# Optimization experiments

Measured on AMD Instinct MI355X. Metric: run time of the kernel, lower is better.

Reference implementation:

```python
import jax, jax.numpy as jnp
import numpy as np
from jax import lax

K = 8            # number of object slots
H = 250          # hidden / fc_size
EPS = 1e-5
DN = ('NCHW', 'OIHW', 'NCHW')


def ln_all(x):
    # F.layer_norm over all non-batch dims, no affine params (torch init: w=1,b=0)
    ax = tuple(range(1, x.ndim))
    m = jnp.mean(x, ax, keepdims=True)
    v = jnp.var(x, ax, keepdims=True)
    return (x - m) * lax.rsqrt(v + EPS)


def ln_last(x):
    # nn.LayerNorm(feat) -> last dim only
    m = jnp.mean(x, -1, keepdims=True)
    v = jnp.var(x, -1, keepdims=True)
    return (x - m) * lax.rsqrt(v + EPS)


def conv(x, w, b):
    # torch Conv2d(k=4, s=2, p=1), NCHW
    y = lax.conv_general_dilated(x, w, (2, 2), [(1, 1), (1, 1)], dimension_numbers=DN)
    return y + b[None, :, None, None]


def up4(x):
    return jnp.repeat(jnp.repeat(x, 4, axis=2), 4, axis=3)


def setup_inputs():
    ks = jax.random.split(jax.random.key(0), 20)
    bk = 48 * K
    p = lambda i, shape, s: jax.random.normal(ks[i], shape, jnp.float32) * s
    z = lambda n: jnp.zeros((n,), jnp.float32)
    return dict(
        x=p(0, (bk, 4096), 1.0),
        state=p(1, (bk, H), 1.0),
        # encoder convs (OIHW) + fc
        c1w=p(2, (16, 1, 4, 4), 0.25), c1b=z(16),
        c2w=p(3, (32, 16, 4, 4), 0.06), c2b=z(32),
        c3w=p(4, (64, 32, 4, 4), 0.04), c3b=z(64),
        efc_w=p(5, (4096, 512), 0.016), efc_b=z(512),
        # R_NEM (weights stored as [in, out])
        renc_w=p(6, (H, H), 0.06), renc_b=z(H),
        core_w=p(7, (2 * H, H), 0.045), core_b=z(H),
        ctx_w=p(8, (H, H), 0.06), ctx_b=z(H),
        att1_w=p(9, (H, 100), 0.06), att1_b=z(100),
        att2_w=p(10, (100, 1), 0.1), att2_b=z(1),
        out_w=p(11, (2 * H + 512, H), 0.03), out_b=z(H),
        # decoder fcs + convs
        dfc1_w=p(12, (H, 512), 0.06), dfc1_b=z(512),
        dfc2_w=p(13, (512, 4096), 0.045), dfc2_b=z(4096),
        d1w=p(14, (32, 64, 4, 4), 0.03), d1b=z(32),
        d2w=p(15, (16, 32, 4, 4), 0.045), d2b=z(16),
        d3w=p(16, (1, 16, 4, 4), 0.06), d3b=z(1),
    )


def reference(x, state, c1w, c1b, c2w, c2b, c3w, c3b, efc_w, efc_b,
              renc_w, renc_b, core_w, core_b, ctx_w, ctx_b,
              att1_w, att1_b, att2_w, att2_b, out_w, out_b,
              dfc1_w, dfc1_b, dfc2_w, dfc2_b, d1w, d1b, d2w, d2b, d3w, d3b):
    bk = x.shape[0]
    b = bk // K

    # ---------------- EncoderLayer ----------------
    def inwrap(h, w, bias):  # InputWrapper conv branch: NHWC -> permute(0,3,2,1) -> conv -> back
        y = conv(jnp.transpose(h, (0, 3, 2, 1)), w, bias)
        return jax.nn.elu(ln_all(jnp.transpose(y, (0, 3, 2, 1))))

    h = x.reshape(bk, 64, 64, 1)
    h = inwrap(h, c1w, c1b)                 # (bk,32,32,16)
    h = inwrap(h, c2w, c2b)                 # (bk,16,16,32)
    h = inwrap(h, c3w, c3b)                 # (bk,8,8,64)
    h = h.reshape(bk, -1)                   # (bk,4096)
    h = jax.nn.elu(ln_last(h @ efc_w + efc_b))   # (bk,512)

    # ---------------- R_NEM (RecurrentLayer) ----------------
    s1 = jax.nn.relu(ln_last(state @ renc_w + renc_b))   # (bk,H)
    s1r = s1.reshape(b, K, H)
    idx = np.array([[j for j in range(K) if j != i] for i in range(K)])  # (K,K-1)
    cs = s1r[:, idx, :]                                    # context: (b,K,K-1,H)
    fs = jnp.broadcast_to(s1r[:, :, None, :], cs.shape)    # focus copies
    pair = jnp.concatenate([fs, cs], axis=-1)              # (b,K,K-1,2H)
    core = jax.nn.relu(ln_last(pair @ core_w + core_b))    # (b,K,K-1,H)
    ctx = jax.nn.relu(ln_last(core @ ctx_w + ctx_b))       # (b,K,K-1,H)
    att = jax.nn.sigmoid(jnp.tanh(ln_last(core @ att1_w + att1_b)) @ att2_w + att2_b)  # (b,K,K-1,1)
    effect = jnp.sum(ctx * att, axis=2).reshape(bk, H)     # attention-weighted sum over K-1
    total = jnp.concatenate([s1, effect, h], axis=1)       # (bk, 2H+512)
    new_state = total @ out_w + out_b                      # (bk,H)
    xr = jax.nn.sigmoid(ln_last(new_state))
    state_out = jax.nn.sigmoid(new_state)

    # ---------------- DecoderLayer ----------------
    d = jax.nn.relu(ln_last(xr @ dfc1_w + dfc1_b))         # (bk,512)
    d = jax.nn.relu(ln_last(d @ dfc2_w + dfc2_b))          # (bk,4096)
    d = d.reshape(bk, 8, 8, 64)

    def outwrap(t, w, bias):
        y = conv(up4(jnp.transpose(t, (0, 3, 2, 1))), w, bias)
        return jnp.transpose(y, (0, 3, 2, 1))

    d = jax.nn.relu(ln_all(outwrap(d, d1w, d1b)))          # (bk,16,16,32)
    d = jax.nn.relu(ln_all(outwrap(d, d2w, d2b)))          # (bk,32,32,16)
    d = jax.nn.sigmoid(outwrap(d, d3w, d3b))               # (bk,64,64,1), no LN
    x_out = d.reshape(bk, -1)                              # (bk,4096)
    return x_out, state_out
```

## Files before the change

### kernel.cpp

```cpp
#include <hip/hip_runtime.h>
#include <hip/hip_bf16.h>
#include <math.h>

typedef __attribute__((ext_vector_type(8))) short bf16x8;
typedef __attribute__((ext_vector_type(4))) float f32x4;

__device__ __forceinline__ float eluf(float v){ return v > 0.f ? v : expm1f(v); }
__device__ __forceinline__ float sigf(float v){ return 1.f/(1.f+expf(-v)); }
__device__ __forceinline__ unsigned short f2bf(float f){
  unsigned u = __float_as_uint(f);
  u += 0x7FFFu + ((u >> 16) & 1u);
  return (unsigned short)(u >> 16);
}
__device__ __forceinline__ float bf2f(short s){
  return __uint_as_float(((unsigned)(unsigned short)s) << 16);
}

__device__ __forceinline__ void block_reduce2(float& a, float& b, float* sbuf){
  __syncthreads();
  for (int off = 32; off; off >>= 1){
    a += __shfl_down(a, off);
    b += __shfl_down(b, off);
  }
  int lane = threadIdx.x & 63, w = threadIdx.x >> 6;
  if (lane == 0){ sbuf[2*w] = a; sbuf[2*w+1] = b; }
  __syncthreads();
  if (threadIdx.x == 0){
    int nw = blockDim.x >> 6;
    float sa = 0.f, sb = 0.f;
    for (int i = 0; i < nw; i++){ sa += sbuf[2*i]; sb += sbuf[2*i+1]; }
    sbuf[0] = sa; sbuf[1] = sb;
  }
  __syncthreads();
  a = sbuf[0]; b = sbuf[1];
}

__device__ __forceinline__ float fold_sum(const float* __restrict__ w, int O, int I,
                                          int o, int i, int pa, int pb, int da, int db){
  float s = 0.f;
  for (int kh = 0; kh < 4; kh++){
    bool inh = (pb==0) ? (db==0 ? (kh==0) : (kh>=1)) : (db==0 ? (kh<=2) : (kh==3));
    if (!inh) continue;
    for (int kw = 0; kw < 4; kw++){
      bool inw = (pa==0) ? (da==0 ? (kw==0) : (kw>=1)) : (da==0 ? (kw<=2) : (kw==3));
      if (!inw) continue;
      s += w[((o*I + i)*4 + kh)*4 + kw];
    }
  }
  return s;
}
__device__ __forceinline__ void fold_elem(const float* __restrict__ w, float* __restrict__ CW,
                                          int O, int I, int l){
  int o = l % O; int q = l / O;
  int da = q & 1, db = (q>>1)&1, pa = (q>>2)&1, pb = (q>>3)&1, i = q>>4;
  CW[(((pb*2+pa)*4 + db*2+da)*I + i)*O + o] = fold_sum(w, O, I, o, i, pa, pb, da, db);
}
__device__ __forceinline__ void cvtc2_elem(const float* __restrict__ w, short* __restrict__ D, int l){
  int i = l & 15, t = (l>>4) & 15, o = l>>8;
  D[l] = (short)f2bf(w[(o*16 + i)*16 + t]);
}
__device__ __forceinline__ void cvtc3_elem(const float* __restrict__ w, short* __restrict__ D, int l){
  int i = l & 31, t = (l>>5) & 15, o = l>>9;
  D[l] = (short)f2bf(w[(o*32 + i)*16 + t]);
}
__device__ __forceinline__ void foldd1_elem(const float* __restrict__ w, short* __restrict__ D, int l){
  int i = l & 63, tap = (l>>6)&3, o = (l>>8)&31, ph = l>>13;
  D[l] = (short)f2bf(fold_sum(w, 32, 64, o, i, ph&1, ph>>1, tap&1, tap>>1));
}
__device__ __forceinline__ void foldd2_elem(const float* __restrict__ w, short* __restrict__ D, int l){
  int i = l & 31, tap = (l>>5)&3, o = (l>>7)&15, ph = l>>11;
  D[l] = (short)f2bf(fold_sum(w, 16, 32, o, i, ph&1, ph>>1, tap&1, tap>>1));
}

__global__ __launch_bounds__(256) void prep_combined(
  const float* __restrict__ efc,  short* __restrict__ Defc,
  const float* __restrict__ dfc2, short* __restrict__ Ddfc2,
  const float* __restrict__ outw, short* __restrict__ Dout,
  const float* __restrict__ corew,short* __restrict__ Dcore,
  const float* __restrict__ dfc1, short* __restrict__ Ddfc1,
  const float* __restrict__ renc, short* __restrict__ Drenc,
  const float* __restrict__ ctx,  const float* __restrict__ att1,
  short* __restrict__ Dctxatt,
  const float* __restrict__ d3w, float* __restrict__ CWT3,
  const float* __restrict__ c2w, short* __restrict__ BtC2,
  const float* __restrict__ c3w, short* __restrict__ BtC3,
  const float* __restrict__ d1w, short* __restrict__ BD1,
  const float* __restrict__ d2w, short* __restrict__ BD2,
  const float* __restrict__ state, short* __restrict__ SBF,
  short* __restrict__ TOTb)
{
  int bx = blockIdx.x;
  if (bx >= 1192){
    const int F3=256, P2=F3+8192, P3=P2+32768, P4=P3+32768, P5=P4+8192,
              ST=P5+98304, TP=ST+4608, TOTAL=TP+8704;
    for (int l = (bx-1192)*256 + threadIdx.x; l < TOTAL; l += 256*256){
      if (l < F3)      fold_elem(d3w, CWT3, 1, 16, l);
      else if (l < P2) cvtc2_elem(c2w, BtC2, l - F3);
      else if (l < P3) cvtc3_elem(c3w, BtC3, l - P2);
      else if (l < P4) foldd1_elem(d1w, BD1, l - P3);
      else if (l < P5) foldd2_elem(d2w, BD2, l - P4);
      else if (l < ST){
        int q = l - P5;
        int n = q >> 8, k = q & 255;
        SBF[q] = (k < 250) ? (short)f2bf(state[n*250 + k]) : (short)0;
      } else if (l < TP){
        int q = l - ST;
        int row = q / 12, cc = q % 12;
        int col = cc < 6 ? 250 + cc : 506 + (cc - 6);
        TOTb[row*1024 + col] = 0;
      } else {
        int q = l - TP;
        int r = q >> 8, cc = q & 255;
        int row = r < 6 ? 250 + r : 356 + (r - 6);
        Dctxatt[row*256 + cc] = 0;
      }
    }
    return;
  }
  const float* W; short* D; int K, N, Kp, base, mode = 0;
  if      (bx < 512) { W=efc;  D=Defc;  K=4096; N=512;  Kp=4096; base=0;    }
  else if (bx < 1024){ W=dfc2; D=Ddfc2; K=512;  N=4096; Kp=512;  base=512;  }
  else if (bx < 1088){ W=outw; D=Dout;  K=1012; N=250;  Kp=1024; base=1024; mode=2; }
  else if (bx < 1120){ W=corew;D=Dcore; K=500;  N=250;  Kp=512;  base=1088; mode=1; }
  else if (bx < 1152){ W=dfc1; D=Ddfc1; K=250;  N=512;  Kp=256;  base=1120; }
  else if (bx < 1168){ W=renc; D=Drenc; K=250;  N=250;  Kp=256;  base=1152; }
  else if (bx < 1184){ W=ctx;  D=Dctxatt;         K=250; N=250; Kp=256; base=1168; }
  else               { W=att1; D=Dctxatt + 65536; K=250; N=100; Kp=256; base=1184; }
  int t = bx - base;
  int tpr = Kp >> 6;
  int tk = t % tpr, tn = t / tpr;
  __shared__ short tile[64][65];
  int c = threadIdx.x & 63, r4 = threadIdx.x >> 6;
  int n0 = tn*64, k0 = tk*64;
  #pragma unroll 4
  for (int p = 0; p < 16; p++){
    int r = r4*16 + p;
    int k = k0 + r, n = n0 + c;
    int ksrc = k; bool valid;
    if (mode == 0) valid = (k < K);
    else if (mode == 1){ valid = (k < 250) || (k >= 256 && k < 506); ksrc = k < 256 ? k : k - 6; }
    else { valid = (k < 250) || (k >= 256 && k < 506) || (k >= 512);
           ksrc = k < 256 ? k : (k < 512 ? k - 6 : k - 12); }
    float v = (valid && n < N) ? W[(size_t)ksrc*N + n] : 0.f;
    tile[c][r] = (short)f2bf(v);
  }
  __syncthreads();
  #pragma unroll 4
  for (int p = 0; p < 16; p++){
    int nn = r4*16 + p;
    int n = n0 + nn;
    if (n < N) D[(size_t)n*Kp + k0 + c] = tile[nn][c];
  }
}

__global__ __launch_bounds__(256) void gemm_mfma(
    const short* __restrict__ Ab, const short* __restrict__ Bt,
    float* __restrict__ P, int M, int N, int Kp, int Kc)
{
  __shared__ __align__(16) short As[64*32];
  __shared__ __align__(16) short Bs[64*32];
  int tid = threadIdx.x;
  int bm = blockIdx.y*64, bn = blockIdx.x*64;
  int kb = blockIdx.z * Kc;
  int kend = kb + Kc;

  int r = tid >> 2, c = tid & 3;
  const short* Arow = Ab + (size_t)(bm + r)*Kp;
  int gn = bn + r;
  bool bval = gn < N;
  const short* Brow = Bt + (size_t)gn*Kp;

  uint4 hA, hB;
  auto load_regs = [&](int k0){
    hA = *(const uint4*)&Arow[k0 + c*8];
    hB = bval ? *(const uint4*)&Brow[k0 + c*8] : make_uint4(0,0,0,0);
  };
  auto write_lds = [&](){
    *(uint4*)&As[r*32 + c*8] = hA;
    *(uint4*)&Bs[r*32 + c*8] = hB;
  };

  int wave = tid >> 6;
  int ln = tid & 15, quad = (tid >> 4) & 3;
  int wr = (wave >> 1) * 32, wc = (wave & 1) * 32;

  f32x4 zero = {0.f, 0.f, 0.f, 0.f};
  f32x4 acc[2][2] = {{zero, zero}, {zero, zero}};

  load_regs(kb);
  write_lds();
  __syncthreads();
  for (int k0 = kb; k0 < kend; k0 += 32){
    int nxt = k0 + 32;
    if (nxt < kend) load_regs(nxt);
    bf16x8 a0 = *(const bf16x8*)&As[(wr +      ln)*32 + quad*8];
    bf16x8 a1 = *(const bf16x8*)&As[(wr + 16 + ln)*32 + quad*8];
    bf16x8 b0 = *(const bf16x8*)&Bs[(wc +      ln)*32 + quad*8];
    bf16x8 b1 = *(const bf16x8*)&Bs[(wc + 16 + ln)*32 + quad*8];
    acc[0][0] = __builtin_amdgcn_mfma_f32_16x16x32_bf16(a0, b0, acc[0][0], 0, 0, 0);
    acc[0][1] = __builtin_amdgcn_mfma_f32_16x16x32_bf16(a0, b1, acc[0][1], 0, 0, 0);
    acc[1][0] = __builtin_amdgcn_mfma_f32_16x16x32_bf16(a1, b0, acc[1][0], 0, 0, 0);
    acc[1][1] = __builtin_amdgcn_mfma_f32_16x16x32_bf16(a1, b1, acc[1][1], 0, 0, 0);
    __syncthreads();
    if (nxt < kend){ write_lds(); __syncthreads(); }
  }

  float* Pout = P + (size_t)blockIdx.z*M*N;
  #pragma unroll
  for (int t = 0; t < 2; t++)
    #pragma unroll
    for (int u = 0; u < 2; u++)
      #pragma unroll
      for (int j = 0; j < 4; j++){
        int row = bm + wr + t*16 + quad*4 + j;
        int col = bn + wc + u*16 + ln;
        if (col < N) Pout[(size_t)row*N + col] = acc[t][u][j];
      }
}

__global__ __launch_bounds__(256) void gemm_conv2g(
    const short* __restrict__ In, const short* __restrict__ Bt,
    short* __restrict__ Out)
{
  __shared__ __align__(16) short As[128*32];
  __shared__ __align__(16) short Bs[32*32];
  int tid = threadIdx.x;
  int bm = blockIdx.x*128;

  int ra = tid >> 1, ca = (tid & 1)*16;
  int gr = bm + ra;
  int n = gr >> 8, pos = gr & 255;
  int oa = pos >> 4, ob = pos & 15;
  const short* ibase = In + (size_t)n*16384;
  int rb = tid >> 2, cb = (tid & 3)*8;
  const short* Brow = Bt + rb*256;
  bool bact = tid < 128;

  uint4 hA0, hA1, hB;
  auto load_regs = [&](int k0){
    #pragma unroll
    for (int h = 0; h < 2; h++){
      int k = k0 + ca + h*8;
      int tap = k >> 4;
      int ai = 2*oa + (tap & 3) - 1, bi = 2*ob + (tap >> 2) - 1;
      bool v = ((unsigned)ai < 32u) && ((unsigned)bi < 32u);
      uint4 tv = v ? *(const uint4*)&ibase[ai*512 + bi*16 + (k & 15)] : make_uint4(0,0,0,0);
      if (h == 0) hA0 = tv; else hA1 = tv;
    }
    if (bact) hB = *(const uint4*)&Brow[k0 + cb];
  };
  auto write_lds = [&](){
    *(uint4*)&As[ra*32 + ca] = hA0;
    *(uint4*)&As[ra*32 + ca + 8] = hA1;
    if (bact) *(uint4*)&Bs[rb*32 + cb] = hB;
  };

  int wave = tid >> 6, ln = tid & 15, quad = (tid >> 4) & 3;
  int wr = wave * 32;

  f32x4 zero = {0.f,0.f,0.f,0.f};
  f32x4 acc[2][2] = {{zero,zero},{zero,zero}};
  load_regs(0); write_lds(); __syncthreads();
  for (int k0 = 0; k0 < 256; k0 += 32){
    int nxt = k0 + 32;
    if (nxt < 256) load_regs(nxt);
    bf16x8 a0 = *(const bf16x8*)&As[(wr +      ln)*32 + quad*8];
    bf16x8 a1 = *(const bf16x8*)&As[(wr + 16 + ln)*32 + quad*8];
    bf16x8 b0 = *(const bf16x8*)&Bs[(     ln)*32 + quad*8];
    bf16x8 b1 = *(const bf16x8*)&Bs[(16 + ln)*32 + quad*8];
    acc[0][0] = __builtin_amdgcn_mfma_f32_16x16x32_bf16(a0, b0, acc[0][0], 0, 0, 0);
    acc[0][1] = __builtin_amdgcn_mfma_f32_16x16x32_bf16(a0, b1, acc[0][1], 0, 0, 0);
    acc[1][0] = __builtin_amdgcn_mfma_f32_16x16x32_bf16(a1, b0, acc[1][0], 0, 0, 0);
    acc[1][1] = __builtin_amdgcn_mfma_f32_16x16x32_bf16(a1, b1, acc[1][1], 0, 0, 0);
    __syncthreads();
    if (nxt < 256){ write_lds(); __syncthreads(); }
  }
  #pragma unroll
  for (int t = 0; t < 2; t++)
    #pragma unroll
    for (int u = 0; u < 2; u++)
      #pragma unroll
      for (int j = 0; j < 4; j++){
        int row = bm + wr + t*16 + quad*4 + j;
        int col = u*16 + ln;
        Out[(size_t)row*32 + col] = (short)f2bf(acc[t][u][j]);
      }
}

__global__ __launch_bounds__(256) void enc_conv3_full(
    const short* __restrict__ E2raw, const float* __restrict__ bias2,
    const short* __restrict__ Bt3, const float* __restrict__ bias3,
    short* __restrict__ outp)
{
  __shared__ __align__(16) short lsamp[18*18*40];
  __shared__ float sbuf[16];
  int n = blockIdx.x, tid = threadIdx.x;
  const short* ip = E2raw + (size_t)n*8192;
  float vv[32];
  float s = 0.f, s2 = 0.f;
  #pragma unroll
  for (int t = 0; t < 4; t++){
    bf16x8 v8 = *(const bf16x8*)&ip[(t*256 + tid)*8];
    #pragma unroll
    for (int j = 0; j < 8; j++){
      int e = (t*256 + tid)*8 + j;
      float v = bf2f(v8[j]) + bias2[e & 31];
      vv[t*8+j] = v; s += v; s2 += v*v;
    }
  }
  block_reduce2(s, s2, sbuf);
  float m2 = s*(1.f/8192.f);
  float rs2 = rsqrtf(s2*(1.f/8192.f) - m2*m2 + 1e-5f);
  for (int l = tid; l < 18*18*40/4; l += 256) ((unsigned long long*)lsamp)[l] = 0ull;
  __syncthreads();
  #pragma unroll
  for (int t = 0; t < 4; t++){
    int e0 = (t*256 + tid)*8;
    int slot = e0 >> 5, ch0 = e0 & 31;
    int a = slot >> 4, b = slot & 15;
    bf16x8 o8;
    #pragma unroll
    for (int j = 0; j < 8; j++)
      o8[j] = (short)f2bf(eluf((vv[t*8+j]-m2)*rs2));
    *(bf16x8*)&lsamp[((a+1)*18 + (b+1))*40 + ch0] = o8;
  }
  int wave = tid>>6, ln = tid&15, quad = (tid>>4)&3;
  int o3 = wave*16 + ln;
  bf16x8 bfr3[16];
  {
    const short* Brow = Bt3 + o3*512;
    #pragma unroll
    for (int ks = 0; ks < 16; ks++)
      bfr3[ks] = *(const bf16x8*)&Brow[ks*32 + quad*8];
  }
  __syncthreads();
  f32x4 z = {0.f,0.f,0.f,0.f};
  f32x4 acc3[4] = {z,z,z,z};
  #pragma unroll
  for (int ks = 0; ks < 16; ks++){
    int kh = ks>>2, kw = ks&3;
    #pragma unroll
    for (int mt = 0; mt < 4; mt++){
      int p = mt*16 + ln;
      int oa = p>>3, ob = p&7;
      bf16x8 a = *(const bf16x8*)&lsamp[((2*oa+kw)*18 + (2*ob+kh))*40 + quad*8];
      acc3[mt] = __builtin_amdgcn_mfma_f32_16x16x32_bf16(a, bfr3[ks], acc3[mt],0,0,0);
    }
  }
  s = 0.f; s2 = 0.f;
  float bz3 = bias3[o3];
  #pragma unroll
  for (int mt = 0; mt < 4; mt++)
    #pragma unroll
    for (int j = 0; j < 4; j++){
      float v = acc3[mt][j] + bz3;
      acc3[mt][j] = v; s += v; s2 += v*v;
    }
  block_reduce2(s, s2, sbuf);
  float m3 = s*(1.f/4096.f);
  float rs3 = rsqrtf(s2*(1.f/4096.f) - m3*m3 + 1e-5f);
  short* op = outp + (size_t)n*4096;
  #pragma unroll
  for (int mt = 0; mt < 4; mt++)
    #pragma unroll
    for (int j = 0; j < 4; j++){
      int p = mt*16 + quad*4 + j;
      int oa = p>>3, ob = p&7;
      op[oa*512 + ob*64 + o3] = f2bf(eluf((acc3[mt][j]-m3)*rs3));
    }
}

__global__ __launch_bounds__(256) void gemm_core_mfma(
    const short* __restrict__ Tb, const short* __restrict__ Bt,
    float* __restrict__ P, int M, int N, int Kc)
{
  __shared__ __align__(16) short As[64*32];
  __shared__ __align__(16) short Bs[64*32];
  int tid = threadIdx.x;
  int bm = blockIdx.y*64, bn = blockIdx.x*64;
  int kb = blockIdx.z * Kc;
  int kend = kb + Kc;

  int r = tid >> 2, c = tid & 3;
  int gr = bm + r;
  int jj2 = gr % 7, fi2 = gr / 7;
  int ii = fi2 & 7, j2 = fi2 >> 3;
  int jidx = jj2 < ii ? jj2 : jj2 + 1;
  const short* own = Tb + (size_t)fi2*1024;
  const short* oth = Tb + (size_t)(j2*8 + jidx)*1024;
  int gn = bn + r;
  bool bval = gn < N;
  const short* Brow = Bt + (size_t)gn*512;

  uint4 hA, hB;
  auto load_regs = [&](int k0){
    int kk = k0 + c*8;
    const short* src = (kk & 256) ? oth : own;
    hA = *(const uint4*)&src[kk & 255];
    hB = bval ? *(const uint4*)&Brow[kk] : make_uint4(0,0,0,0);
  };
  auto write_lds = [&](){
    *(uint4*)&As[r*32 + c*8] = hA;
    *(uint4*)&Bs[r*32 + c*8] = hB;
  };

  int wave = tid >> 6;
  int ln = tid & 15, quad = (tid >> 4) & 3;
  int wr = (wave >> 1) * 32, wc = (wave & 1) * 32;

  f32x4 zero = {0.f, 0.f, 0.f, 0.f};
  f32x4 acc[2][2] = {{zero, zero}, {zero, zero}};

  load_regs(kb);
  write_lds();
  __syncthreads();
  for (int k0 = kb; k0 < kend; k0 += 32){
    int nxt = k0 + 32;
    if (nxt < kend) load_regs(nxt);
    bf16x8 a0 = *(const bf16x8*)&As[(wr +      ln)*32 + quad*8];
    bf16x8 a1 = *(const bf16x8*)&As[(wr + 16 + ln)*32 + quad*8];
    bf16x8 b0 = *(const bf16x8*)&Bs[(wc +      ln)*32 + quad*8];
    bf16x8 b1 = *(const bf16x8*)&Bs[(wc + 16 + ln)*32 + quad*8];
    acc[0][0] = __builtin_amdgcn_mfma_f32_16x16x32_bf16(a0, b0, acc[0][0], 0, 0, 0);
    acc[0][1] = __builtin_amdgcn_mfma_f32_16x16x32_bf16(a0, b1, acc[0][1], 0, 0, 0);
    acc[1][0] = __builtin_amdgcn_mfma_f32_16x16x32_bf16(a1, b0, acc[1][0], 0, 0, 0);
    acc[1][1] = __builtin_amdgcn_mfma_f32_16x16x32_bf16(a1, b1, acc[1][1], 0, 0, 0);
    __syncthreads();
    if (nxt < kend){ write_lds(); __syncthreads(); }
  }

  float* Pout = P + (size_t)blockIdx.z*M*N;
  #pragma unroll
  for (int t = 0; t < 2; t++)
    #pragma unroll
    for (int u = 0; u < 2; u++)
      #pragma unroll
      for (int j = 0; j < 4; j++){
        int row = bm + wr + t*16 + quad*4 + j;
        int col = bn + wc + u*16 + ln;
        if (col < N) Pout[(size_t)row*N + col] = acc[t][u][j];
      }
}

__global__ __launch_bounds__(256) void reduce_ln(
    const float* __restrict__ Pp, const float* __restrict__ bias,
    void* __restrict__ outp, int M, int N, int KS, int os, int act, int obf, int bmask)
{
  __shared__ float rowbuf[4096];
  __shared__ float sbuf[16];
  int row = blockIdx.x;
  size_t MN = (size_t)M*N;
  float s = 0.f, s2 = 0.f;
  for (int c = threadIdx.x; c < N; c += 256){
    float v = bias[c & bmask];
    for (int ks = 0; ks < KS; ks++) v += Pp[ks*MN + (size_t)row*N + c];
    rowbuf[c] = v; s += v; s2 += v*v;
  }
  block_reduce2(s, s2, sbuf);
  float m = s / N;
  float r = rsqrtf(s2/N - m*m + 1e-5f);
  for (int c = threadIdx.x; c < N; c += 256){
    float v = (rowbuf[c]-m)*r;
    if (act == 1) v = fmaxf(v, 0.f);
    else if (act == 2) v = eluf(v);
    else if (act == 3) v = tanhf(v);
    if (obf) ((short*)outp)[(size_t)row*os + c] = f2bf(v);
    else     ((float*)outp)[(size_t)row*os + c] = v;
  }
}

__global__ __launch_bounds__(256) void reduce_ns(
    const float* __restrict__ Pp, const float* __restrict__ bias,
    short* __restrict__ XRb, float* __restrict__ so, int M, int N, int KS)
{
  __shared__ float rowbuf[256];
  __shared__ float sbuf[16];
  int row = blockIdx.x;
  size_t MN = (size_t)M*N;
  float s = 0.f, s2 = 0.f;
  for (int c = threadIdx.x; c < N; c += 256){
    float v = bias[c];
    for (int ks = 0; ks < KS; ks++) v += Pp[ks*MN + (size_t)row*N + c];
    rowbuf[c] = v; s += v; s2 += v*v;
  }
  block_reduce2(s, s2, sbuf);
  float m = s / N;
  float r = rsqrtf(s2/N - m*m + 1e-5f);
  for (int c = threadIdx.x; c < N; c += 256){
    float v = rowbuf[c];
    XRb[(size_t)row*256 + c] = f2bf(sigf((v-m)*r));
    so[(size_t)row*N + c] = sigf(v);
  }
}

__global__ __launch_bounds__(448) void ctx_att_effect(
    const float* __restrict__ Pc, const float* __restrict__ ctx_b,
    const float* __restrict__ att1_b,
    const float* __restrict__ w2, const float* __restrict__ b2,
    short* __restrict__ tot)
{
  __shared__ float ctxs[7][250];
  __shared__ float att_s[7];
  int fi = blockIdx.x, tid = threadIdx.x;
  int jj = tid >> 6, lane = tid & 63;
  const size_t MN = (size_t)2688*384;
  int row = fi*7 + jj;
  float vv[4];
  float s = 0.f, s2 = 0.f;
  #pragma unroll
  for (int t = 0; t < 4; t++){
    int c = lane + t*64;
    float v = 0.f;
    if (c < 250) v = ctx_b[c] + Pc[(size_t)row*384 + c] + Pc[MN + (size_t)row*384 + c];
    vv[t] = v; s += v; s2 += v*v;
  }
  #pragma unroll
  for (int off = 32; off; off >>= 1){ s += __shfl_down(s, off); s2 += __shfl_down(s2, off); }
  s = __shfl(s, 0); s2 = __shfl(s2, 0);
  float m = s*(1.f/250.f);
  float r = rsqrtf(s2*(1.f/250.f) - m*m + 1e-5f);
  #pragma unroll
  for (int t = 0; t < 4; t++){
    int c = lane + t*64;
    if (c < 250) ctxs[jj][c] = fmaxf((vv[t]-m)*r, 0.f);
  }
  float va[2];
  s = 0.f; s2 = 0.f;
  #pragma unroll
  for (int t = 0; t < 2; t++){
    int c = lane + t*64;
    float v = 0.f;
    if (c < 100)
      v = att1_b[c] + Pc[(size_t)row*384 + 256 + c] + Pc[MN + (size_t)row*384 + 256 + c];
    va[t] = v; s += v; s2 += v*v;
  }
  #pragma unroll
  for (int off = 32; off; off >>= 1){ s += __shfl_down(s, off); s2 += __shfl_down(s2, off); }
  s = __shfl(s, 0); s2 = __shfl(s2, 0);
  m = s*0.01f;
  r = rsqrtf(s2*0.01f - m*m + 1e-5f);
  float d = 0.f;
  #pragma unroll
  for (int t = 0; t < 2; t++){
    int c = lane + t*64;
    if (c < 100) d += tanhf((va[t]-m)*r)*w2[c];
  }
  #pragma unroll
  for (int off = 32; off; off >>= 1) d += __shfl_down(d, off);
  if (lane == 0) att_s[jj] = sigf(d + b2[0]);
  __syncthreads();
  for (int h = tid; h < 250; h += 448){
    float sum = 0.f;
    #pragma unroll
    for (int q = 0; q < 7; q++) sum += ctxs[q][h]*att_s[q];
    tot[(size_t)fi*1024 + 256 + h] = f2bf(sum);
  }
}

__global__ __launch_bounds__(256) void enc_conv1_ig(
    const float* __restrict__ x, const float* __restrict__ w, const float* __restrict__ bias,
    short* __restrict__ outp)
{
  __shared__ __align__(16) float in_t[66*68];
  __shared__ short rawb[16384];
  __shared__ float sbuf[16];
  int n = blockIdx.x, tid = threadIdx.x;
  for (int l = tid; l < 66*68; l += 256) in_t[l] = 0.f;
  __syncthreads();
  const float* xin = x + (size_t)n*4096;
  for (int l4 = tid; l4 < 1024; l4 += 256){
    float4 v = *(const float4*)&xin[l4*4];
    int aa = (l4*4) >> 6, bb = (l4*4) & 63;
    float* dst = &in_t[(aa+1)*68 + bb + 1];
    dst[0]=v.x; dst[1]=v.y; dst[2]=v.z; dst[3]=v.w;
  }
  int o = tid & 15;
  float wr[16];
  #pragma unroll
  for (int t = 0; t < 16; t++) wr[t] = w[o*16 + t];
  float bv = bias[o];
  __syncthreads();
  float s = 0.f, s2 = 0.f;
  for (int r = 0; r < 64; r++){
    int idx = tid + (r<<8);
    int bq = (idx>>4)&31, aq = idx>>9;
    int a0 = 2*aq, b0 = 2*bq;
    float acc = bv;
    #pragma unroll
    for (int kw = 0; kw < 4; kw++){
      const float* row = &in_t[(a0+kw)*68 + b0];
      float2 p0 = *(const float2*)&row[0];
      float2 p1 = *(const float2*)&row[2];
      acc += p0.x*wr[0*4+kw] + p0.y*wr[1*4+kw] + p1.x*wr[2*4+kw] + p1.y*wr[3*4+kw];
    }
    rawb[idx] = f2bf(acc);
    s += acc; s2 += acc*acc;
  }
  block_reduce2(s, s2, sbuf);
  float m = s*(1.f/16384.f);
  float rs = rsqrtf(s2*(1.f/16384.f) - m*m + 1e-5f);
  short* op = outp + (size_t)n*16384;
  for (int l = tid; l < 16384; l += 256){
    float v = bf2f(rawb[l]);
    op[l] = f2bf(eluf((v-m)*rs));
  }
}

__global__ __launch_bounds__(256) void dec_conv12_mfma(
    const short* __restrict__ in, const short* __restrict__ Bd1, const float* __restrict__ bias1,
    const short* __restrict__ Bd2, const float* __restrict__ bias2, short* __restrict__ outp)
{
  __shared__ __align__(16) short smem[18*18*40];
  __shared__ float sbuf[16];
  int n = blockIdx.x, tid = threadIdx.x;
  for (int l = tid; l < 1800; l += 256) ((unsigned long long*)smem)[l] = 0ull;
  __syncthreads();
  const short* ip = in + (size_t)n*4096;
  for (int l = tid; l < 1024; l += 256){
    int i4 = l & 15, sb = (l>>4)&7, sa = l>>7;
    *(uint2*)&smem[((sa+1)*10 + (sb+1))*72 + i4*4] = *(const uint2*)&ip[sa*512 + sb*64 + i4*4];
  }
  int wave = tid>>6, ln = tid&15, quad = (tid>>4)&3;
  int pa = wave & 1, pb = wave >> 1;
  bf16x8 bfr1[2][8];
  #pragma unroll
  for (int nt = 0; nt < 2; nt++){
    const short* Brow = Bd1 + (wave*32 + nt*16 + ln)*256;
    #pragma unroll
    for (int ks = 0; ks < 8; ks++)
      bfr1[nt][ks] = *(const bf16x8*)&Brow[ks*32 + quad*8];
  }
  __syncthreads();
  f32x4 z = {0.f,0.f,0.f,0.f};
  f32x4 acc[2][4] = {{z,z,z,z},{z,z,z,z}};
  #pragma unroll
  for (int ks = 0; ks < 8; ks++){
    int tap = ks>>1, ibase = (ks&1)*32 + quad*8;
    int da = tap & 1, db = tap >> 1;
    #pragma unroll
    for (int mt = 0; mt < 4; mt++){
      int p = mt*16 + ln;
      int ta = p>>3, tb = p&7;
      bf16x8 a = *(const bf16x8*)&smem[((ta+da+pa)*10 + (tb+db+pb))*72 + ibase];
      acc[0][mt] = __builtin_amdgcn_mfma_f32_16x16x32_bf16(a, bfr1[0][ks], acc[0][mt],0,0,0);
      acc[1][mt] = __builtin_amdgcn_mfma_f32_16x16x32_bf16(a, bfr1[1][ks], acc[1][mt],0,0,0);
    }
  }
  float s = 0.f, s2 = 0.f;
  #pragma unroll
  for (int nt = 0; nt < 2; nt++){
    float bz = bias1[nt*16 + ln];
    #pragma unroll
    for (int mt = 0; mt < 4; mt++)
      #pragma unroll
      for (int j = 0; j < 4; j++){
        float v = acc[nt][mt][j] + bz;
        acc[nt][mt][j] = v; s += v; s2 += v*v;
      }
  }
  block_reduce2(s, s2, sbuf);
  float m1 = s*(1.f/8192.f);
  float rs1 = rsqrtf(s2*(1.f/8192.f) - m1*m1 + 1e-5f);
  bf16x8 bfr2[4];
  {
    const short* Brow = Bd2 + (wave*16 + ln)*128;
    #pragma unroll
    for (int ks = 0; ks < 4; ks++)
      bfr2[ks] = *(const bf16x8*)&Brow[ks*32 + quad*8];
  }
  for (int l = tid; l < 3240; l += 256) ((unsigned long long*)smem)[l] = 0ull;
  __syncthreads();
  #pragma unroll
  for (int nt = 0; nt < 2; nt++){
    int o = nt*16 + ln;
    #pragma unroll
    for (int mt = 0; mt < 4; mt++)
      #pragma unroll
      for (int j = 0; j < 4; j++){
        int p = mt*16 + quad*4 + j;
        int ta = p>>3, tb = p&7;
        int sa = 2*ta + pa, sb = 2*tb + pb;
        smem[((sa+1)*18 + (sb+1))*40 + o] = f2bf(fmaxf((acc[nt][mt][j]-m1)*rs1, 0.f));
      }
  }
  __syncthreads();
  f32x4 acc2[16] = {z,z,z,z,z,z,z,z,z,z,z,z,z,z,z,z};
  #pragma unroll
  for (int ks = 0; ks < 4; ks++){
    int da = ks & 1, db = ks >> 1;
    #pragma unroll
    for (int mt = 0; mt < 16; mt++){
      int p = mt*16 + ln;
      int ta = p>>4, tb = p&15;
      bf16x8 a = *(const bf16x8*)&smem[((ta+da+pa)*18 + (tb+db+pb))*40 + quad*8];
      acc2[mt] = __builtin_amdgcn_mfma_f32_16x16x32_bf16(a, bfr2[ks], acc2[mt],0,0,0);
    }
  }
  s = 0.f; s2 = 0.f;
  float bz2 = bias2[ln];
  #pragma unroll
  for (int mt = 0; mt < 16; mt++)
    #pragma unroll
    for (int j = 0; j < 4; j++){
      float v = acc2[mt][j] + bz2;
      acc2[mt][j] = v; s += v; s2 += v*v;
    }
  block_reduce2(s, s2, sbuf);
  float m = s*(1.f/16384.f);
  float rs = rsqrtf(s2*(1.f/16384.f) - m*m + 1e-5f);
  short* op = outp + (size_t)n*16384;
  #pragma unroll
  for (int mt = 0; mt < 16; mt++)
    #pragma unroll
    for (int j = 0; j < 4; j++){
      int p = mt*16 + quad*4 + j;
      int ta = p>>4, tb = p&15;
      op[(2*ta+pa)*512 + (2*tb+pb)*16 + ln] = f2bf(fmaxf((acc2[mt][j]-m)*rs, 0.f));
    }
}

__global__ __launch_bounds__(256) void dec_conv3_ig(
    const short* __restrict__ in, const float* __restrict__ CWT, const float* __restrict__ bias,
    float* __restrict__ outp)
{
  __shared__ __align__(16) float in_t[9792];
  __shared__ __align__(16) float wl[256];
  int bx = blockIdx.x;
  int n = bx >> 1, b0 = (bx & 1) * 32, tb0 = b0 >> 1;
  int tid = threadIdx.x;
  const short* ip = in + (size_t)n*16384;
  for (int l = tid; l < 9792; l += 256){
    int i = l & 15, sb = (l >> 4) % 18, sap = l / 288;
    int sa = sap - 1, sbg = tb0 - 1 + sb;
    float v = 0.f;
    if ((unsigned)sa < 32u && (unsigned)sbg < 32u)
      v = bf2f(ip[sa*512 + sbg*16 + i]);
    in_t[(sap*18 + sb)*16 + i] = v;
  }
  for (int l = tid; l < 256; l += 256) wl[l] = CWT[l];
  __syncthreads();
  float bv = bias[0];
  int bl = tid & 31, ath = tid >> 5;
  int b = b0 + bl;
  int tb = b >> 1, pb = b & 1;
  float* op = outp + (size_t)n*4096;
  #pragma unroll
  for (int j = 0; j < 8; j++){
    int a = ath*8 + j;
    int ta = a >> 1, pa = a & 1;
    float4 s4 = make_float4(0.f,0.f,0.f,0.f);
    #pragma unroll
    for (int db = 0; db < 2; db++){
      int sb = tb + db + (pb ? 0 : -1);
      int sbl = sb - (tb0 - 1);
      #pragma unroll
      for (int da = 0; da < 2; da++){
        int sa = ta + da + (pa ? 0 : -1);
        int sap = sa + 1;
        const float4* A4 = (const float4*)&in_t[(sap*18 + sbl)*16];
        const float4* B4 = (const float4*)&wl[((pb*2+pa)*4 + db*2+da)*16];
        #pragma unroll
        for (int q = 0; q < 4; q++){
          float4 av = A4[q], bw = B4[q];
          s4.x += av.x*bw.x; s4.y += av.y*bw.y;
          s4.z += av.z*bw.z; s4.w += av.w*bw.w;
        }
      }
    }
    op[a*64 + b] = sigf(bv + s4.x + s4.y + s4.z + s4.w);
  }
}

extern "C" void kernel_launch(void* const* d_in, const int* in_sizes, int n_in,
                              void* d_out, int out_size, void* d_ws, size_t ws_size,
                              hipStream_t stream) {
  const float* x      = (const float*)d_in[0];
  const float* state  = (const float*)d_in[1];
  const float* c1w    = (const float*)d_in[2];
  const float* c1b    = (const float*)d_in[3];
  const float* c2w    = (const float*)d_in[4];
  const float* c2b    = (const float*)d_in[5];
  const float* c3w    = (const float*)d_in[6];
  const float* c3b    = (const float*)d_in[7];
  const float* efc_w  = (const float*)d_in[8];
  const float* efc_b  = (const float*)d_in[9];
  const float* renc_w = (const float*)d_in[10];
  const float* renc_b = (const float*)d_in[11];
  const float* core_w = (const float*)d_in[12];
  const float* core_b = (const float*)d_in[13];
  const float* ctx_w  = (const float*)d_in[14];
  const float* ctx_b  = (const float*)d_in[15];
  const float* att1_w = (const float*)d_in[16];
  const float* att1_b = (const float*)d_in[17];
  const float* att2_w = (const float*)d_in[18];
  const float* att2_b = (const float*)d_in[19];
  const float* out_w  = (const float*)d_in[20];
  const float* out_b  = (const float*)d_in[21];
  const float* dfc1_w = (const float*)d_in[22];
  const float* dfc1_b = (const float*)d_in[23];
  const float* dfc2_w = (const float*)d_in[24];
  const float* dfc2_b = (const float*)d_in[25];
  const float* d1w    = (const float*)d_in[26];
  const float* d1b    = (const float*)d_in[27];
  const float* d2w    = (const float*)d_in[28];
  const float* d2b    = (const float*)d_in[29];
  const float* d3w    = (const float*)d_in[30];
  const float* d3b    = (const float*)d_in[31];

  float* wsf = (float*)d_ws;
  size_t o = 0;
  float* PB   = wsf + o; o += (size_t)2112*1024;
  float* CWT3 = wsf + o; o += 256;
  short* E1b  = (short*)(wsf + o); o += (size_t)384*16384/2;
  short* E2b  = (short*)(wsf + o); o += (size_t)384*8192/2;
  short* E3b  = (short*)(wsf + o); o += (size_t)384*4096/2;
  short* TOTb = (short*)(wsf + o); o += (size_t)384*1024/2;
  short* C1b  = (short*)(wsf + o); o += (size_t)2688*256/2;
  short* XRb  = (short*)(wsf + o); o += (size_t)384*256/2;
  short* G1b  = (short*)(wsf + o); o += (size_t)384*512/2;
  short* SBF  = (short*)(wsf + o); o += (size_t)384*256/2;
  short* BtC2 = (short*)(wsf + o); o += 8192/2;
  short* BtC3 = (short*)(wsf + o); o += 32768/2;
  short* BD1  = (short*)(wsf + o); o += 32768/2;
  short* BD2  = (short*)(wsf + o); o += 8192/2;
  short* BT_efc    = (short*)(wsf + o); o += 2097152/2;
  short* BT_renc   = (short*)(wsf + o); o += 64000/2;
  short* BT_core   = (short*)(wsf + o); o += 128000/2;
  short* BT_ctxatt = (short*)(wsf + o); o += 98304/2;
  short* BT_out    = (short*)(wsf + o); o += 256000/2;
  short* BT_dfc1   = (short*)(wsf + o); o += 131072/2;
  short* BT_dfc2   = (short*)(wsf + o); o += 2097152/2;
  short* D2b = E1b;
  short* G2b = E3b;

  float* xout = (float*)d_out;
  float* sout = xout + (size_t)384*4096;

  prep_combined<<<1448, 256, 0, stream>>>(
      efc_w, BT_efc, dfc2_w, BT_dfc2, out_w, BT_out, core_w, BT_core,
      dfc1_w, BT_dfc1, renc_w, BT_renc, ctx_w, att1_w, BT_ctxatt,
      d3w, CWT3, c2w, BtC2, c3w, BtC3, d1w, BD1, d2w, BD2, state, SBF, TOTb);

  enc_conv1_ig<<<384, 256, 0, stream>>>(x, c1w, c1b, E1b);
  gemm_conv2g<<<768, 256, 0, stream>>>(E1b, BtC2, E2b);
  enc_conv3_full<<<384, 256, 0, stream>>>(E2b, c2b, BtC3, c3b, E3b);
  gemm_mfma<<<dim3(8,6,8), 256, 0, stream>>>(E3b, BT_efc, PB, 384, 512, 4096, 512);
  reduce_ln<<<384, 256, 0, stream>>>(PB, efc_b, TOTb+512, 384, 512, 8, 1024, 2, 1, -1);

  gemm_mfma<<<dim3(4,6,8), 256, 0, stream>>>(SBF, BT_renc, PB, 384, 250, 256, 32);
  reduce_ln<<<384, 256, 0, stream>>>(PB, renc_b, TOTb, 384, 250, 8, 1024, 1, 1, -1);
  gemm_core_mfma<<<dim3(4,42,2), 256, 0, stream>>>(TOTb, BT_core, PB, 2688, 250, 256);
  reduce_ln<<<2688, 256, 0, stream>>>(PB, core_b, C1b, 2688, 250, 2, 256, 1, 1, -1);
  gemm_mfma<<<dim3(6,42,2), 256, 0, stream>>>(C1b, BT_ctxatt, PB, 2688, 384, 256, 128);
  ctx_att_effect<<<384, 448, 0, stream>>>(PB, ctx_b, att1_b, att2_w, att2_b, TOTb);

  gemm_mfma<<<dim3(4,6,8), 256, 0, stream>>>(TOTb, BT_out, PB, 384, 250, 1024, 128);
  reduce_ns<<<384, 256, 0, stream>>>(PB, out_b, XRb, sout, 384, 250, 8);

  gemm_mfma<<<dim3(8,6,4), 256, 0, stream>>>(XRb, BT_dfc1, PB, 384, 512, 256, 64);
  reduce_ln<<<384, 256, 0, stream>>>(PB, dfc1_b, G1b, 384, 512, 4, 512, 1, 1, -1);
  gemm_mfma<<<dim3(64,6,1), 256, 0, stream>>>(G1b, BT_dfc2, PB, 384, 4096, 512, 512);
  reduce_ln<<<384, 256, 0, stream>>>(PB, dfc2_b, G2b, 384, 4096, 1, 4096, 1, 1, -1);

  dec_conv12_mfma<<<384, 256, 0, stream>>>(G2b, BD1, d1b, BD2, d2b, D2b);
  dec_conv3_ig<<<768, 256, 0, stream>>>(D2b, CWT3, d3b, xout);

  (void)in_sizes; (void)n_in; (void)out_size; (void)ws_size;
}
```

Before: 322.3 us.

## Co-schedule independent encoder and relational stages in shared fused launches

Turns the encoder conv chain and the R_NEM relational GEMM/layernorm chain into device bodies. Independent stages from the two chains are now interleaved into five combined kernels that branch on block index, for example conv1 with the renc GEMM and conv2 with the renc layernorm. Each stage now writes its own partial-sum buffer so concurrent stages cannot clobber each other. This removes several launches and fills the GPU with work from both branches. The cost is that each combined kernel's LDS and register footprint is the maximum of its branches, which may lower occupancy, and the workspace grows.

```diff
diff --git a/kernel.cpp b/kernel.cpp
--- a/kernel.cpp
+++ b/kernel.cpp
@@ -153,15 +153,16 @@
   }
 }
 
-__global__ __launch_bounds__(256) void gemm_mfma(
+__device__ __forceinline__ void gemm_body(
     const short* __restrict__ Ab, const short* __restrict__ Bt,
-    float* __restrict__ P, int M, int N, int Kp, int Kc)
+    float* __restrict__ P, int M, int N, int Kp, int Kc,
+    int bxx, int byy, int bzz)
 {
   __shared__ __align__(16) short As[64*32];
   __shared__ __align__(16) short Bs[64*32];
   int tid = threadIdx.x;
-  int bm = blockIdx.y*64, bn = blockIdx.x*64;
-  int kb = blockIdx.z * Kc;
+  int bm = byy*64, bn = bxx*64;
+  int kb = bzz * Kc;
   int kend = kb + Kc;
 
   int r = tid >> 2, c = tid & 3;
@@ -205,7 +206,7 @@
     if (nxt < kend){ write_lds(); __syncthreads(); }
   }
 
-  float* Pout = P + (size_t)blockIdx.z*M*N;
+  float* Pout = P + (size_t)bzz*M*N;
   #pragma unroll
   for (int t = 0; t < 2; t++)
     #pragma unroll
@@ -218,14 +219,21 @@
       }
 }
 
-__global__ __launch_bounds__(256) void gemm_conv2g(
+__global__ __launch_bounds__(256) void gemm_mfma(
+    const short* __restrict__ Ab, const short* __restrict__ Bt,
+    float* __restrict__ P, int M, int N, int Kp, int Kc)
+{
+  gemm_body(Ab, Bt, P, M, N, Kp, Kc, blockIdx.x, blockIdx.y, blockIdx.z);
+}
+
+__device__ __forceinline__ void conv2g_body(
     const short* __restrict__ In, const short* __restrict__ Bt,
-    short* __restrict__ Out)
+    short* __restrict__ Out, int bxx)
 {
   __shared__ __align__(16) short As[128*32];
   __shared__ __align__(16) short Bs[32*32];
   int tid = threadIdx.x;
-  int bm = blockIdx.x*128;
+  int bm = bxx*128;
 
   int ra = tid >> 1, ca = (tid & 1)*16;
   int gr = bm + ra;
@@ -287,14 +295,14 @@
       }
 }
 
-__global__ __launch_bounds__(256) void enc_conv3_full(
+__device__ __forceinline__ void conv3_full_body(
     const short* __restrict__ E2raw, const float* __restrict__ bias2,
     const short* __restrict__ Bt3, const float* __restrict__ bias3,
-    short* __restrict__ outp)
+    short* __restrict__ outp, int n)
 {
   __shared__ __align__(16) short lsamp[18*18*40];
   __shared__ float sbuf[16];
-  int n = blockIdx.x, tid = threadIdx.x;
+  int tid = threadIdx.x;
   const short* ip = E2raw + (size_t)n*8192;
   float vv[32];
   float s = 0.f, s2 = 0.f;
@@ -370,15 +378,16 @@
     }
 }
 
-__global__ __launch_bounds__(256) void gemm_core_mfma(
+__device__ __forceinline__ void gemm_core_body(
     const short* __restrict__ Tb, const short* __restrict__ Bt,
-    float* __restrict__ P, int M, int N, int Kc)
+    float* __restrict__ P, int M, int N, int Kc,
+    int bxx, int byy, int bzz)
 {
   __shared__ __align__(16) short As[64*32];
   __shared__ __align__(16) short Bs[64*32];
   int tid = threadIdx.x;
-  int bm = blockIdx.y*64, bn = blockIdx.x*64;
-  int kb = blockIdx.z * Kc;
+  int bm = byy*64, bn = bxx*64;
+  int kb = bzz * Kc;
   int kend = kb + Kc;
 
   int r = tid >> 2, c = tid & 3;
@@ -429,7 +438,7 @@
     if (nxt < kend){ write_lds(); __syncthreads(); }
   }
 
-  float* Pout = P + (size_t)blockIdx.z*M*N;
+  float* Pout = P + (size_t)bzz*M*N;
   #pragma unroll
   for (int t = 0; t < 2; t++)
     #pragma unroll
@@ -442,13 +451,13 @@
       }
 }
 
-__global__ __launch_bounds__(256) void reduce_ln(
+__device__ __forceinline__ void reduce_ln_body(
     const float* __restrict__ Pp, const float* __restrict__ bias,
-    void* __restrict__ outp, int M, int N, int KS, int os, int act, int obf, int bmask)
+    void* __restrict__ outp, int M, int N, int KS, int os, int act, int obf, int bmask,
+    int row)
 {
   __shared__ float rowbuf[4096];
   __shared__ float sbuf[16];
-  int row = blockIdx.x;
   size_t MN = (size_t)M*N;
   float s = 0.f, s2 = 0.f;
   for (int c = threadIdx.x; c < N; c += 256){
@@ -469,6 +478,126 @@
   }
 }
 
+__global__ __launch_bounds__(256) void reduce_ln(
+    const float* __restrict__ Pp, const float* __restrict__ bias,
+    void* __restrict__ outp, int M, int N, int KS, int os, int act, int obf, int bmask)
+{
+  reduce_ln_body(Pp, bias, outp, M, N, KS, os, act, obf, bmask, blockIdx.x);
+}
+
+__device__ __forceinline__ void enc_conv1_body(
+    const float* __restrict__ x, const float* __restrict__ w, const float* __restrict__ bias,
+    short* __restrict__ outp, int n)
+{
+  __shared__ __align__(16) float in_t[66*68];
+  __shared__ short rawb[16384];
+  __shared__ float sbuf[16];
+  int tid = threadIdx.x;
+  for (int l = tid; l < 66*68; l += 256) in_t[l] = 0.f;
+  __syncthreads();
+  const float* xin = x + (size_t)n*4096;
+  for (int l4 = tid; l4 < 1024; l4 += 256){
+    float4 v = *(const float4*)&xin[l4*4];
+    int aa = (l4*4) >> 6, bb = (l4*4) & 63;
+    float* dst = &in_t[(aa+1)*68 + bb + 1];
+    dst[0]=v.x; dst[1]=v.y; dst[2]=v.z; dst[3]=v.w;
+  }
+  int o = tid & 15;
+  float wr[16];
+  #pragma unroll
+  for (int t = 0; t < 16; t++) wr[t] = w[o*16 + t];
+  float bv = bias[o];
+  __syncthreads();
+  float s = 0.f, s2 = 0.f;
+  for (int r = 0; r < 64; r++){
+    int idx = tid + (r<<8);
+    int bq = (idx>>4)&31, aq = idx>>9;
+    int a0 = 2*aq, b0 = 2*bq;
+    float acc = bv;
+    #pragma unroll
+    for (int kw = 0; kw < 4; kw++){
+      const float* row = &in_t[(a0+kw)*68 + b0];
+      float2 p0 = *(const float2*)&row[0];
+      float2 p1 = *(const float2*)&row[2];
+      acc += p0.x*wr[0*4+kw] + p0.y*wr[1*4+kw] + p1.x*wr[2*4+kw] + p1.y*wr[3*4+kw];
+    }
+    rawb[idx] = f2bf(acc);
+    s += acc; s2 += acc*acc;
+  }
+  block_reduce2(s, s2, sbuf);
+  float m = s*(1.f/16384.f);
+  float rs = rsqrtf(s2*(1.f/16384.f) - m*m + 1e-5f);
+  short* op = outp + (size_t)n*16384;
+  for (int l = tid; l < 16384; l += 256){
+    float v = bf2f(rawb[l]);
+    op[l] = f2bf(eluf((v-m)*rs));
+  }
+}
+
+__global__ __launch_bounds__(256) void fuse_a(
+    const float* __restrict__ x, const float* __restrict__ c1w, const float* __restrict__ c1b,
+    short* __restrict__ E1b,
+    const short* __restrict__ SBF, const short* __restrict__ BT_renc, float* __restrict__ PB_renc)
+{
+  int b = blockIdx.x;
+  if (b < 384){
+    enc_conv1_body(x, c1w, c1b, E1b, b);
+  } else {
+    int id = b - 384;
+    gemm_body(SBF, BT_renc, PB_renc, 384, 250, 256, 32, id & 3, (id >> 2) % 6, id / 24);
+  }
+}
+
+__global__ __launch_bounds__(256) void fuse_b(
+    const float* __restrict__ PB_renc, const float* __restrict__ renc_b, short* __restrict__ TOTb,
+    const short* __restrict__ E1b, const short* __restrict__ BtC2, short* __restrict__ E2b)
+{
+  int b = blockIdx.x;
+  if (b < 384){
+    reduce_ln_body(PB_renc, renc_b, TOTb, 384, 250, 8, 1024, 1, 1, -1, b);
+  } else {
+    conv2g_body(E1b, BtC2, E2b, b - 384);
+  }
+}
+
+__global__ __launch_bounds__(256) void fuse_c(
+    const short* __restrict__ TOTb, const short* __restrict__ BT_core, float* __restrict__ PB_core,
+    const short* __restrict__ E2b, const float* __restrict__ c2b,
+    const short* __restrict__ BtC3, const float* __restrict__ c3b, short* __restrict__ E3b)
+{
+  int b = blockIdx.x;
+  if (b < 336){
+    gemm_core_body(TOTb, BT_core, PB_core, 2688, 250, 256, b % 4, (b / 4) % 42, b / 168);
+  } else {
+    conv3_full_body(E2b, c2b, BtC3, c3b, E3b, b - 336);
+  }
+}
+
+__global__ __launch_bounds__(256) void fuse_d(
+    const float* __restrict__ PB_core, const float* __restrict__ core_b, short* __restrict__ C1b,
+    const short* __restrict__ E3b, const short* __restrict__ BT_efc, float* __restrict__ PB_efc)
+{
+  int b = blockIdx.x;
+  if (b < 2688){
+    reduce_ln_body(PB_core, core_b, C1b, 2688, 250, 2, 256, 1, 1, -1, b);
+  } else {
+    int id = b - 2688;
+    gemm_body(E3b, BT_efc, PB_efc, 384, 512, 4096, 512, id & 7, (id >> 3) % 6, id / 48);
+  }
+}
+
+__global__ __launch_bounds__(256) void fuse_e(
+    const short* __restrict__ C1b, const short* __restrict__ BT_ctxatt, float* __restrict__ PB_ctxatt,
+    const float* __restrict__ PB_efc, const float* __restrict__ efc_b, short* __restrict__ TOTh)
+{
+  int b = blockIdx.x;
+  if (b < 504){
+    gemm_body(C1b, BT_ctxatt, PB_ctxatt, 2688, 384, 256, 128, b % 6, (b / 6) % 42, b / 252);
+  } else {
+    reduce_ln_body(PB_efc, efc_b, TOTh, 384, 512, 8, 1024, 2, 1, -1, b - 504);
+  }
+}
+
 __global__ __launch_bounds__(256) void reduce_ns(
     const float* __restrict__ Pp, const float* __restrict__ bias,
     short* __restrict__ XRb, float* __restrict__ so, int M, int N, int KS)
@@ -554,55 +683,6 @@
     #pragma unroll
     for (int q = 0; q < 7; q++) sum += ctxs[q][h]*att_s[q];
     tot[(size_t)fi*1024 + 256 + h] = f2bf(sum);
-  }
-}
-
-__global__ __launch_bounds__(256) void enc_conv1_ig(
-    const float* __restrict__ x, const float* __restrict__ w, const float* __restrict__ bias,
-    short* __restrict__ outp)
-{
-  __shared__ __align__(16) float in_t[66*68];
-  __shared__ short rawb[16384];
-  __shared__ float sbuf[16];
-  int n = blockIdx.x, tid = threadIdx.x;
-  for (int l = tid; l < 66*68; l += 256) in_t[l] = 0.f;
-  __syncthreads();
-  const float* xin = x + (size_t)n*4096;
-  for (int l4 = tid; l4 < 1024; l4 += 256){
-    float4 v = *(const float4*)&xin[l4*4];
-    int aa = (l4*4) >> 6, bb = (l4*4) & 63;
-    float* dst = &in_t[(aa+1)*68 + bb + 1];
-    dst[0]=v.x; dst[1]=v.y; dst[2]=v.z; dst[3]=v.w;
-  }
-  int o = tid & 15;
-  float wr[16];
-  #pragma unroll
-  for (int t = 0; t < 16; t++) wr[t] = w[o*16 + t];
-  float bv = bias[o];
-  __syncthreads();
-  float s = 0.f, s2 = 0.f;
-  for (int r = 0; r < 64; r++){
-    int idx = tid + (r<<8);
-    int bq = (idx>>4)&31, aq = idx>>9;
-    int a0 = 2*aq, b0 = 2*bq;
-    float acc = bv;
-    #pragma unroll
-    for (int kw = 0; kw < 4; kw++){
-      const float* row = &in_t[(a0+kw)*68 + b0];
-      float2 p0 = *(const float2*)&row[0];
-      float2 p1 = *(const float2*)&row[2];
-      acc += p0.x*wr[0*4+kw] + p0.y*wr[1*4+kw] + p1.x*wr[2*4+kw] + p1.y*wr[3*4+kw];
-    }
-    rawb[idx] = f2bf(acc);
-    s += acc; s2 += acc*acc;
-  }
-  block_reduce2(s, s2, sbuf);
-  float m = s*(1.f/16384.f);
-  float rs = rsqrtf(s2*(1.f/16384.f) - m*m + 1e-5f);
-  short* op = outp + (size_t)n*16384;
-  for (int l = tid; l < 16384; l += 256){
-    float v = bf2f(rawb[l]);
-    op[l] = f2bf(eluf((v-m)*rs));
   }
 }
 
@@ -809,7 +889,13 @@
 
   float* wsf = (float*)d_ws;
   size_t o = 0;
-  float* PB   = wsf + o; o += (size_t)2112*1024;
+  float* PB_renc   = wsf + o; o += (size_t)8*384*250;
+  float* PB_core   = wsf + o; o += (size_t)2*2688*250;
+  float* PB_efc    = wsf + o; o += (size_t)8*384*512;
+  float* PB_ctxatt = wsf + o; o += (size_t)2*2688*384;
+  float* PB_out    = wsf + o; o += (size_t)8*384*250;
+  float* PB_dfc1   = wsf + o; o += (size_t)4*384*512;
+  float* PB_dfc2   = wsf + o; o += (size_t)384*4096;
   float* CWT3 = wsf + o; o += 256;
   short* E1b  = (short*)(wsf + o); o += (size_t)384*16384/2;
   short* E2b  = (short*)(wsf + o); o += (size_t)384*8192/2;
@@ -841,26 +927,21 @@
       dfc1_w, BT_dfc1, renc_w, BT_renc, ctx_w, att1_w, BT_ctxatt,
       d3w, CWT3, c2w, BtC2, c3w, BtC3, d1w, BD1, d2w, BD2, state, SBF, TOTb);
 
-  enc_conv1_ig<<<384, 256, 0, stream>>>(x, c1w, c1b, E1b);
-  gemm_conv2g<<<768, 256, 0, stream>>>(E1b, BtC2, E2b);
-  enc_conv3_full<<<384, 256, 0, stream>>>(E2b, c2b, BtC3, c3b, E3b);
-  gemm_mfma<<<dim3(8,6,8), 256, 0, stream>>>(E3b, BT_efc, PB, 384, 512, 4096, 512);
-  reduce_ln<<<384, 256, 0, stream>>>(PB, efc_b, TOTb+512, 384, 512, 8, 1024, 2, 1, -1);
-
-  gemm_mfma<<<dim3(4,6,8), 256, 0, stream>>>(SBF, BT_renc, PB, 384, 250, 256, 32);
-  reduce_ln<<<384, 256, 0, stream>>>(PB, renc_b, TOTb, 384, 250, 8, 1024, 1, 1, -1);
-  gemm_core_mfma<<<dim3(4,42,2), 256, 0, stream>>>(TOTb, BT_core, PB, 2688, 250, 256);
-  reduce_ln<<<2688, 256, 0, stream>>>(PB, core_b, C1b, 2688, 250, 2, 256, 1, 1, -1);
-  gemm_mfma<<<dim3(6,42,2), 256, 0, stream>>>(C1b, BT_ctxatt, PB, 2688, 384, 256, 128);
-  ctx_att_effect<<<384, 448, 0, stream>>>(PB, ctx_b, att1_b, att2_w, att2_b, TOTb);
-
-  gemm_mfma<<<dim3(4,6,8), 256, 0, stream>>>(TOTb, BT_out, PB, 384, 250, 1024, 128);
-  reduce_ns<<<384, 256, 0, stream>>>(PB, out_b, XRb, sout, 384, 250, 8);
-
-  gemm_mfma<<<dim3(8,6,4), 256, 0, stream>>>(XRb, BT_dfc1, PB, 384, 512, 256, 64);
-  reduce_ln<<<384, 256, 0, stream>>>(PB, dfc1_b, G1b, 384, 512, 4, 512, 1, 1, -1);
-  gemm_mfma<<<dim3(64,6,1), 256, 0, stream>>>(G1b, BT_dfc2, PB, 384, 4096, 512, 512);
-  reduce_ln<<<384, 256, 0, stream>>>(PB, dfc2_b, G2b, 384, 4096, 1, 4096, 1, 1, -1);
+  fuse_a<<<576, 256, 0, stream>>>(x, c1w, c1b, E1b, SBF, BT_renc, PB_renc);
+  fuse_b<<<1152, 256, 0, stream>>>(PB_renc, renc_b, TOTb, E1b, BtC2, E2b);
+  fuse_c<<<720, 256, 0, stream>>>(TOTb, BT_core, PB_core, E2b, c2b, BtC3, c3b, E3b);
+  fuse_d<<<3072, 256, 0, stream>>>(PB_core, core_b, C1b, E3b, BT_efc, PB_efc);
+  fuse_e<<<888, 256, 0, stream>>>(C1b, BT_ctxatt, PB_ctxatt, PB_efc, efc_b, TOTb+512);
+
+  ctx_att_effect<<<384, 448, 0, stream>>>(PB_ctxatt, ctx_b, att1_b, att2_w, att2_b, TOTb);
+
+  gemm_mfma<<<dim3(4,6,8), 256, 0, stream>>>(TOTb, BT_out, PB_out, 384, 250, 1024, 128);
+  reduce_ns<<<384, 256, 0, stream>>>(PB_out, out_b, XRb, sout, 384, 250, 8);
+
+  gemm_mfma<<<dim3(8,6,4), 256, 0, stream>>>(XRb, BT_dfc1, PB_dfc1, 384, 512, 256, 64);
+  reduce_ln<<<384, 256, 0, stream>>>(PB_dfc1, dfc1_b, G1b, 384, 512, 4, 512, 1, 1, -1);
+  gemm_mfma<<<dim3(64,6,1), 256, 0, stream>>>(G1b, BT_dfc2, PB_dfc2, 384, 4096, 512, 512);
+  reduce_ln<<<384, 256, 0, stream>>>(PB_dfc2, dfc2_b, G2b, 384, 4096, 1, 4096, 1, 1, -1);
 
   dec_conv12_mfma<<<384, 256, 0, stream>>>(G2b, BD1, d1b, BD2, d2b, D2b);
   dec_conv3_ig<<<768, 256, 0, stream>>>(D2b, CWT3, d3b, xout);
```

Result: faster. 293.7 us (-8.9%).
